# Kernel optimization log

Hardware: AMD Instinct MI355X
Metric: run time of the kernel (lower is better)

The kernel has to match this reference:

```python
import jax, jax.numpy as jnp
import numpy as np

D_MODEL = 1024
NUM_HEADS = 16
D_K = D_MODEL // NUM_HEADS
D_FF = 4096
LN_EPS = 1e-5


def layer_norm(x, gamma, beta):
    mu = jnp.mean(x, axis=-1, keepdims=True)
    var = jnp.var(x, axis=-1, keepdims=True)
    return (x - mu) * jax.lax.rsqrt(var + LN_EPS) * gamma + beta


def setup_inputs() -> dict:
    key = jax.random.key(0)
    ks = jax.random.split(key, 10)
    s = 0.02
    return {
        "x": jax.random.normal(ks[0], (2, 2048, D_MODEL), dtype=jnp.float32),
        # per-head projections stacked: [H, d_model, d_k] (equivalent to the
        # num_heads separate nn.Linear(d_model, d_k, bias=False) modules)
        "Wq": jax.random.normal(ks[1], (NUM_HEADS, D_MODEL, D_K), dtype=jnp.float32) * s,
        "Wk": jax.random.normal(ks[2], (NUM_HEADS, D_MODEL, D_K), dtype=jnp.float32) * s,
        "Wv": jax.random.normal(ks[3], (NUM_HEADS, D_MODEL, D_K), dtype=jnp.float32) * s,
        "Wo": jax.random.normal(ks[4], (D_MODEL, D_MODEL), dtype=jnp.float32) * s,
        "W1": jax.random.normal(ks[5], (D_MODEL, D_FF), dtype=jnp.float32) * s,
        "b1": jnp.zeros((D_FF,), dtype=jnp.float32),
        "W2": jax.random.normal(ks[6], (D_FF, D_MODEL), dtype=jnp.float32) * s,
        "b2": jnp.zeros((D_MODEL,), dtype=jnp.float32),
        "g1": jnp.ones((D_MODEL,), dtype=jnp.float32),
        "beta1": jnp.zeros((D_MODEL,), dtype=jnp.float32),
        "g2": jnp.ones((D_MODEL,), dtype=jnp.float32),
        "beta2": jnp.zeros((D_MODEL,), dtype=jnp.float32),
    }


def reference(x, Wq, Wk, Wv, Wo, W1, b1, W2, b2, g1, beta1, g2, beta2):
    B, S, D = x.shape
    # ---- pre-LN multi-head self-attention ----
    h = layer_norm(x, g1, beta1)
    # batched QKV projections (equivalent to the per-head Python loop)
    Q = jnp.einsum('bsd,hdk->bhsk', h, Wq)  # [B,H,S,dk]
    K = jnp.einsum('bsd,hdk->bhsk', h, Wk)
    V = jnp.einsum('bsd,hdk->bhsk', h, Wv)
    scores = jnp.einsum('bhqk,bhsk->bhqs', Q, K) / jnp.sqrt(jnp.asarray(D_K, x.dtype))
    weights = jax.nn.softmax(scores, axis=-1)  # [B,H,S,S]
    attn = jnp.einsum('bhqs,bhsk->bhqk', weights, V)  # [B,H,S,dk]
    # concat heads along feature dim (head order preserved)
    concat = attn.transpose(0, 2, 1, 3).reshape(B, S, D)
    x = x + concat @ Wo
    # ---- pre-LN FFN (exact erf GELU, matching nn.GELU default) ----
    h2 = layer_norm(x, g2, beta2)
    ffn = jax.nn.gelu(h2 @ W1 + b1, approximate=False) @ W2 + b2
    return x + ffn
```

## Files before the change

### kernel.cpp

```cpp
#include <hip/hip_runtime.h>
#include <stdint.h>


typedef __attribute__((ext_vector_type(8))) short bf16x8;
typedef __attribute__((ext_vector_type(4))) float f32x4;
typedef __attribute__((ext_vector_type(16))) float f32x16;
typedef __attribute__((ext_vector_type(4))) unsigned short u16x4;
typedef __attribute__((ext_vector_type(4))) unsigned int u32x4;

#define DEV __device__ __forceinline__

static constexpr int DM   = 1024;
static constexpr int DFF  = 4096;
static constexpr int NH   = 16;
static constexpr int DKH  = 64;
static constexpr int SEQ  = 2048;
static constexpr int NBAT = 2;
static constexpr int NTOK = NBAT * SEQ;

DEV unsigned short f2bf(float f) {
  union { float f; unsigned int u; } v; v.f = f;
  unsigned int u = v.u;
  return (unsigned short)((u + 0x7fffu + ((u >> 16) & 1u)) >> 16);
}

DEV void gload_lds16(const unsigned short* g, unsigned short* l) {
  __builtin_amdgcn_global_load_lds(
      (const __attribute__((address_space(1))) unsigned int*)g,
      (__attribute__((address_space(3))) unsigned int*)l, 16, 0, 0);
}

DEV float fast_gelu(float x) {
  const float z = fabsf(x) * 0.70710678118654752f;
  const float t = __builtin_amdgcn_rcpf(1.0f + 0.3275911f * z);
  float p = 1.061405429f;
  p = p * t - 1.453152027f;
  p = p * t + 1.421413741f;
  p = p * t - 0.284496736f;
  p = p * t + 0.254829592f;
  p = p * t;
  float erfv = 1.0f - p * __expf(-z * z);
  erfv = copysignf(erfv, x);
  return 0.5f * x * (1.0f + erfv);
}

__global__ __launch_bounds__(256) void ln_kernel(
    const float* __restrict__ x, const float* __restrict__ g,
    const float* __restrict__ be, unsigned short* __restrict__ out) {
  const int row = blockIdx.x;
  const int t = threadIdx.x;
  const int lane = t & 63, w = t >> 6;
  const float4* xr = (const float4*)(x + (size_t)row * DM);
  float4 v = xr[t];
  float s  = v.x + v.y + v.z + v.w;
  float s2 = v.x * v.x + v.y * v.y + v.z * v.z + v.w * v.w;
#pragma unroll
  for (int off = 32; off; off >>= 1) {
    s  += __shfl_down(s, off);
    s2 += __shfl_down(s2, off);
  }
  __shared__ float rs_[4], rq_[4];
  if (lane == 0) { rs_[w] = s; rq_[w] = s2; }
  __syncthreads();
  float fs = rs_[0] + rs_[1] + rs_[2] + rs_[3];
  float fq = rq_[0] + rq_[1] + rq_[2] + rq_[3];
  float mu = fs * (1.0f / DM);
  float var = fq * (1.0f / DM) - mu * mu;
  float rstd = rsqrtf(var + 1e-5f);
  float4 gv = ((const float4*)g)[t];
  float4 bv = ((const float4*)be)[t];
  u16x4 o;
  o[0] = f2bf((v.x - mu) * rstd * gv.x + bv.x);
  o[1] = f2bf((v.y - mu) * rstd * gv.y + bv.y);
  o[2] = f2bf((v.z - mu) * rstd * gv.z + bv.z);
  o[3] = f2bf((v.w - mu) * rstd * gv.w + bv.w);
  *(u16x4*)(out + (size_t)row * DM + t * 4) = o;
}

__global__ __launch_bounds__(256) void transpose_weights(
    const float* __restrict__ Wq, const float* __restrict__ Wk,
    const float* __restrict__ Wv, const float* __restrict__ Wo,
    const float* __restrict__ W1, const float* __restrict__ W2,
    unsigned short* __restrict__ wqkv_t, unsigned short* __restrict__ wo_t,
    unsigned short* __restrict__ w1_t, unsigned short* __restrict__ w2_t) {
  __shared__ float lds[64][65];
  const int t = blockIdx.x;
  const float* inb; unsigned short* outb; int in_ld, out_ld;
  if (t < 768) {
    const int slice = t >> 4, tin = t & 15;
    const int which = slice >> 4, h = slice & 15;
    const float* W = (which == 0) ? Wq : (which == 1) ? Wk : Wv;
    inb = W + (size_t)((h << 10) + (tin << 6)) * 64;
    in_ld = 64;
    outb = wqkv_t + ((size_t)((which << 10) + (h << 6)) << 10) + (tin << 6);
    out_ld = 1024;
  } else if (t < 1024) {
    const int tt = t - 768, tr = tt >> 4, tc = tt & 15;
    inb = Wo + (size_t)(tc << 6) * 1024 + (tr << 6); in_ld = 1024;
    outb = wo_t + (size_t)(tr << 6) * 1024 + (tc << 6); out_ld = 1024;
  } else if (t < 2048) {
    const int tt = t - 1024, tr = tt >> 4, tc = tt & 15;
    inb = W1 + (size_t)(tc << 6) * 4096 + (tr << 6); in_ld = 4096;
    outb = w1_t + (size_t)(tr << 6) * 1024 + (tc << 6); out_ld = 1024;
  } else {
    const int tt = t - 2048, tr = tt >> 6, tc = tt & 63;
    inb = W2 + (size_t)(tc << 6) * 1024 + (tr << 6); in_ld = 1024;
    outb = w2_t + (size_t)(tr << 6) * 4096 + (tc << 6); out_ld = 4096;
  }
  const int j = threadIdx.x & 63, i0 = threadIdx.x >> 6;
#pragma unroll
  for (int p = 0; p < 16; ++p) {
    const int i = i0 + p * 4;
    lds[j][i] = inb[(size_t)i * in_ld + j];
  }
  __syncthreads();
#pragma unroll
  for (int p = 0; p < 16; ++p) {
    const int r = i0 + p * 4;
    outb[(size_t)r * out_ld + j] = f2bf(lds[r][j]);
  }
}

struct EpiArgs {
  unsigned short* q;
  unsigned short* k;
  unsigned short* vt;
  unsigned short* ob16;
  float* of32;
  float* p0;
  const float* bias;
  const float* resid;
};

template <int EPI>
DEV void epilogue_elem(float v, int row, int col, int N, int bz,
                       const EpiArgs& ep) {
  if constexpr (EPI == 0) {
    const int bb = row >> 11, rr = row & 2047;
    if (col < 1024) {
      const int hh = col >> 6, dk = col & 63;
      const int kk = dk >> 4, h8 = (dk >> 3) & 1, e = dk & 7;
      const int qblk = rr >> 5, l31 = rr & 31;
      ep.q[((size_t)(bb * NH + hh) * 64 + qblk) * 2048 + kk * 512 +
           (h8 * 32 + l31) * 8 + e] = f2bf(v * 0.18033688011112042f);
    } else if (col < 2048) {
      const int c = col - 1024;
      const int hh = c >> 6, dk = c & 63;
      const int kk = dk >> 4, h8 = (dk >> 3) & 1, e = dk & 7;
      const int kvblk = rr >> 5, l31 = rr & 31;
      ep.k[((size_t)(bb * NH + hh) * 64 + kvblk) * 2048 + kk * 512 +
           (h8 * 32 + l31) * 8 + e] = f2bf(v);
    } else {
      const int c = col - 2048, hh = c >> 6, dd = c & 63;
      const int ssw = (rr & ~12) | ((rr & 4) << 1) | ((rr & 8) >> 1);
      const int t64 = ssw >> 6, w = (ssw >> 4) & 3;
      const int h8 = (ssw >> 3) & 1, e = ssw & 7;
      const int dblk = dd >> 5, l31 = dd & 31;
      ep.vt[(((size_t)(bb * NH + hh) * 32 + t64) * 8 + dblk * 4 + w) * 512 +
            (h8 * 32 + l31) * 8 + e] = f2bf(v);
    }
  } else if constexpr (EPI == 1) {
    const size_t idx = (size_t)row * N + col;
    ep.of32[idx] = v + ep.resid[idx];
  } else if constexpr (EPI == 2) {
    ep.ob16[(size_t)row * N + col] = f2bf(fast_gelu(v + ep.bias[col]));
  } else {
    const size_t idx = (size_t)row * N + col;
    if (bz == 0) ep.p0[idx] = v;
    else ep.of32[idx] = ep.of32[idx] + v + ep.bias[col];
  }
}

template <int EPI>
__global__ __launch_bounds__(512, 2) void gemm_256(
    const unsigned short* __restrict__ A, const unsigned short* __restrict__ Bt,
    int N, int K, int ldk, EpiArgs ep) {
  __shared__ __align__(16) unsigned short Als[2][256 * 64];
  __shared__ __align__(16) unsigned short Bls[2][256 * 64];
  const int t = threadIdx.x, lane = t & 63, wave = t >> 6;
  const int wm = wave >> 2, wn = wave & 3;
  const int g = lane >> 4, r16 = lane & 15;
  const int nx = gridDim.x, nwg = nx * gridDim.y;
  int wgid = blockIdx.y * nx + blockIdx.x;
  wgid = (wgid & 7) * (nwg >> 3) + (wgid >> 3);
  const int m0 = (wgid / nx) * 256, n0 = (wgid % nx) * 256;

  f32x4 acc[8][4];
  const f32x4 z4 = {0.f, 0.f, 0.f, 0.f};
#pragma unroll
  for (int i = 0; i < 8; ++i)
#pragma unroll
    for (int j = 0; j < 4; ++j) acc[i][j] = z4;

  auto stage_half = [&](int b, int k0, int h) {
#pragma unroll
    for (int i = 0; i < 2; ++i) {
      const int c = i * 512 + t;
      const int row = c >> 3;
      const int sc = ((c & 7) ^ (row & 7)) * 8;
      const int dofs = ((h & 1) << 13) + (i * 512 + (wave << 6)) * 8;
      if (h < 2)
        gload_lds16(A + (size_t)(m0 + ((h & 1) << 7) + row) * ldk + k0 + sc,
                    &Als[b][dofs]);
      else
        gload_lds16(Bt + (size_t)(n0 + ((h & 1) << 7) + row) * ldk + k0 + sc,
                    &Bls[b][dofs]);
    }
  };

  const int NT = K >> 6;
#pragma unroll
  for (int h = 0; h < 4; ++h) stage_half(0, 0, h);

  for (int kt = 0; kt < NT; ++kt) {
    const int cur = kt & 1;
    const bool more = (kt + 1) < NT;
    const int nk0 = (kt + 1) << 6;
    __builtin_amdgcn_s_barrier();
    if (more) {
      stage_half(cur ^ 1, nk0, 0);
      stage_half(cur ^ 1, nk0, 1);
      asm volatile("s_waitcnt vmcnt(4)" ::: "memory");
    } else {
      asm volatile("s_waitcnt vmcnt(0)" ::: "memory");
    }
    __builtin_amdgcn_s_barrier();
    __builtin_amdgcn_sched_barrier(0);

    bf16x8 Af[8][2];
#pragma unroll
    for (int mf = 0; mf < 8; ++mf) {
      const int row = (wm << 7) + (mf << 4) + r16;
#pragma unroll
      for (int ks = 0; ks < 2; ++ks)
        Af[mf][ks] = *(const bf16x8*)
            &Als[cur][row * 64 + ((((ks << 2) | g) ^ (row & 7)) << 3)];
    }
#pragma unroll
    for (int qn = 0; qn < 2; ++qn) {
      bf16x8 Bf[2][2];
#pragma unroll
      for (int ni = 0; ni < 2; ++ni) {
        const int row = (wn << 6) + (((qn << 1) | ni) << 4) + r16;
#pragma unroll
        for (int ks = 0; ks < 2; ++ks)
          Bf[ni][ks] = *(const bf16x8*)
              &Bls[cur][row * 64 + ((((ks << 2) | g) ^ (row & 7)) << 3)];
      }
      __builtin_amdgcn_s_setprio(1);
#pragma unroll
      for (int ks = 0; ks < 2; ++ks)
#pragma unroll
        for (int mf = 0; mf < 8; ++mf)
#pragma unroll
          for (int ni = 0; ni < 2; ++ni)
            acc[mf][(qn << 1) | ni] = __builtin_amdgcn_mfma_f32_16x16x32_bf16(
                Af[mf][ks], Bf[ni][ks], acc[mf][(qn << 1) | ni], 0, 0, 0);
      __builtin_amdgcn_s_setprio(0);
      if (qn == 0 && more) {
        stage_half(cur ^ 1, nk0, 2);
        stage_half(cur ^ 1, nk0, 3);
      }
    }
  }
#pragma unroll
  for (int mf = 0; mf < 8; ++mf)
#pragma unroll
    for (int nf = 0; nf < 4; ++nf)
#pragma unroll
      for (int r = 0; r < 4; ++r)
        epilogue_elem<EPI>(acc[mf][nf][r],
                           m0 + (wm << 7) + (mf << 4) + (g << 2) + r,
                           n0 + (wn << 6) + (nf << 4) + r16, N, 0, ep);
}

template <int EPI>
__global__ __launch_bounds__(256) void gemm_pipe(
    const unsigned short* __restrict__ A, const unsigned short* __restrict__ Bt,
    int N, int Kc, int ldk, EpiArgs ep) {
  __shared__ __align__(16) unsigned short Als[2][128 * 64];
  __shared__ __align__(16) unsigned short Bls[2][128 * 64];
  const int t = threadIdx.x, lane = t & 63, wave = t >> 6;
  const int wm = wave >> 1, wn = wave & 1;
  const int g = lane >> 4, r16 = lane & 15;
  const int nx = gridDim.x;
  const int nwg = nx * gridDim.y;
  int wgid = blockIdx.y * nx + blockIdx.x;
  wgid = (wgid & 7) * (nwg >> 3) + (wgid >> 3);
  const int m0 = (wgid / nx) * 128, n0 = (wgid % nx) * 128;
  const int kbase = blockIdx.z * Kc;

  f32x4 acc[4][4];
  const f32x4 z4 = {0.f, 0.f, 0.f, 0.f};
#pragma unroll
  for (int i = 0; i < 4; ++i)
#pragma unroll
    for (int j = 0; j < 4; ++j) acc[i][j] = z4;

  auto stage = [&](int b, int k0) {
#pragma unroll
    for (int i = 0; i < 4; ++i) {
      const int cb = i * 256 + wave * 64;
      const int c = cb + lane;
      const int row = c >> 3;
      const int sc = ((c & 7) ^ (row & 7)) * 8;
      gload_lds16(A + (size_t)(m0 + row) * ldk + kbase + k0 + sc, &Als[b][cb * 8]);
      gload_lds16(Bt + (size_t)(n0 + row) * ldk + kbase + k0 + sc, &Bls[b][cb * 8]);
    }
  };

  const int NT = Kc >> 6;
  stage(0, 0);
  for (int kt = 0; kt < NT; ++kt) {
    const int cur = kt & 1;
    __builtin_amdgcn_s_barrier();
    if (kt + 1 < NT) {
      stage(cur ^ 1, (kt + 1) << 6);
      asm volatile("s_waitcnt vmcnt(8)" ::: "memory");
    } else {
      asm volatile("s_waitcnt vmcnt(0)" ::: "memory");
    }
    __builtin_amdgcn_s_barrier();
    __builtin_amdgcn_sched_barrier(0);

    const int sw = r16 & 7;
    bf16x8 af[2][4], bfr[2][4];
#pragma unroll
    for (int ks = 0; ks < 2; ++ks) {
#pragma unroll
      for (int mt = 0; mt < 4; ++mt)
        af[ks][mt] = *(const bf16x8*)&Als[cur][(wm * 64 + mt * 16 + r16) * 64 +
                                              (((ks << 2) | g) ^ sw) * 8];
#pragma unroll
      for (int nt = 0; nt < 4; ++nt)
        bfr[ks][nt] = *(const bf16x8*)&Bls[cur][(wn * 64 + nt * 16 + r16) * 64 +
                                               (((ks << 2) | g) ^ sw) * 8];
    }
    __builtin_amdgcn_s_setprio(1);
#pragma unroll
    for (int ks = 0; ks < 2; ++ks)
#pragma unroll
      for (int mt = 0; mt < 4; ++mt)
#pragma unroll
        for (int nt = 0; nt < 4; ++nt)
          acc[mt][nt] = __builtin_amdgcn_mfma_f32_16x16x32_bf16(
              af[ks][mt], bfr[ks][nt], acc[mt][nt], 0, 0, 0);
    __builtin_amdgcn_s_setprio(0);
  }
#pragma unroll
  for (int mt = 0; mt < 4; ++mt)
#pragma unroll
    for (int nt = 0; nt < 4; ++nt)
#pragma unroll
      for (int r = 0; r < 4; ++r)
        epilogue_elem<EPI>(acc[mt][nt][r], m0 + wm * 64 + mt * 16 + g * 4 + r,
                           n0 + wn * 64 + nt * 16 + r16, N, blockIdx.z, ep);
}

__global__ __launch_bounds__(256) void reduce_add(const float* __restrict__ p,
                                                  float* __restrict__ out) {
  const int i = blockIdx.x * 256 + threadIdx.x;
  float4 a = ((const float4*)p)[i];
  float4 b = ((float4*)out)[i];
  b.x += a.x; b.y += a.y; b.z += a.z; b.w += a.w;
  ((float4*)out)[i] = b;
}

struct AttnState {
  f32x16 o0, o1;
  float m, lsum;
};

DEV void load_k(const unsigned short* kbase, int s, bf16x8 k0[4], bf16x8 k1[4]) {
  const unsigned short* p = kbase + (size_t)(s >> 5) * 2048;
#pragma unroll
  for (int kk = 0; kk < 4; ++kk) {
    k0[kk] = *(const bf16x8*)(p + kk * 512);
    k1[kk] = *(const bf16x8*)(p + 2048 + kk * 512);
  }
}

DEV void attn_tile(const bf16x8 k0[4], const bf16x8 k1[4],
                   const bf16x8 v0[4], const bf16x8 v1[4],
                   const bf16x8 qf[4], AttnState& st) {
  const f32x16 z16 = {0.f};
  f32x16 pA = z16, pB = z16;
  __builtin_amdgcn_s_setprio(1);
#pragma unroll
  for (int kk = 0; kk < 4; ++kk) {
    pA = __builtin_amdgcn_mfma_f32_32x32x16_bf16(k0[kk], qf[kk], pA, 0, 0, 0);
    pB = __builtin_amdgcn_mfma_f32_32x32x16_bf16(k1[kk], qf[kk], pB, 0, 0, 0);
  }
  __builtin_amdgcn_s_setprio(0);
  float m0 = fmaxf(pA[0], pB[0]), m1 = fmaxf(pA[1], pB[1]);
  float m2 = fmaxf(pA[2], pB[2]), m3 = fmaxf(pA[3], pB[3]);
#pragma unroll
  for (int r = 4; r < 16; r += 4) {
    m0 = fmaxf(m0, fmaxf(pA[r + 0], pB[r + 0]));
    m1 = fmaxf(m1, fmaxf(pA[r + 1], pB[r + 1]));
    m2 = fmaxf(m2, fmaxf(pA[r + 2], pB[r + 2]));
    m3 = fmaxf(m3, fmaxf(pA[r + 3], pB[r + 3]));
  }
  float mx = fmaxf(fmaxf(m0, m1), fmaxf(m2, m3));
  mx = fmaxf(mx, __shfl_xor(mx, 32));
  if (__any(mx > st.m + 11.5416f)) {
    const float mnew = fmaxf(st.m, mx);
    const float corr = __builtin_amdgcn_exp2f(st.m - mnew);
#pragma unroll
    for (int r = 0; r < 16; ++r) { st.o0[r] *= corr; st.o1[r] *= corr; }
    st.lsum *= corr;
    st.m = mnew;
  }
  float ps = 0.f;
#pragma unroll
  for (int r = 0; r < 16; ++r) {
    pA[r] = __builtin_amdgcn_exp2f(pA[r] - st.m); ps += pA[r];
    pB[r] = __builtin_amdgcn_exp2f(pB[r] - st.m); ps += pB[r];
  }
  ps += __shfl_xor(ps, 32);
  st.lsum += ps;
  bf16x8 pw[4];
#pragma unroll
  for (int w = 0; w < 4; ++w) {
    unsigned int wd0, wd1, wd2, wd3;
    const int e0 = (w & 1) * 8;
    if (w < 2) {
      asm("v_cvt_pk_bf16_f32 %0, %1, %2" : "=v"(wd0) : "v"(pA[e0 + 0]), "v"(pA[e0 + 1]));
      asm("v_cvt_pk_bf16_f32 %0, %1, %2" : "=v"(wd1) : "v"(pA[e0 + 2]), "v"(pA[e0 + 3]));
      asm("v_cvt_pk_bf16_f32 %0, %1, %2" : "=v"(wd2) : "v"(pA[e0 + 4]), "v"(pA[e0 + 5]));
      asm("v_cvt_pk_bf16_f32 %0, %1, %2" : "=v"(wd3) : "v"(pA[e0 + 6]), "v"(pA[e0 + 7]));
    } else {
      asm("v_cvt_pk_bf16_f32 %0, %1, %2" : "=v"(wd0) : "v"(pB[e0 + 0]), "v"(pB[e0 + 1]));
      asm("v_cvt_pk_bf16_f32 %0, %1, %2" : "=v"(wd1) : "v"(pB[e0 + 2]), "v"(pB[e0 + 3]));
      asm("v_cvt_pk_bf16_f32 %0, %1, %2" : "=v"(wd2) : "v"(pB[e0 + 4]), "v"(pB[e0 + 5]));
      asm("v_cvt_pk_bf16_f32 %0, %1, %2" : "=v"(wd3) : "v"(pB[e0 + 6]), "v"(pB[e0 + 7]));
    }
    u32x4 wv = {wd0, wd1, wd2, wd3};
    pw[w] = __builtin_bit_cast(bf16x8, wv);
  }
  __builtin_amdgcn_s_setprio(1);
#pragma unroll
  for (int w = 0; w < 4; ++w) {
    st.o0 = __builtin_amdgcn_mfma_f32_32x32x16_bf16(v0[w], pw[w], st.o0, 0, 0, 0);
    st.o1 = __builtin_amdgcn_mfma_f32_32x32x16_bf16(v1[w], pw[w], st.o1, 0, 0, 0);
  }
  __builtin_amdgcn_s_setprio(0);
}

__global__ __launch_bounds__(256, 2) void attn_kernel(
    const unsigned short* __restrict__ Qc, const unsigned short* __restrict__ Kc,
    const unsigned short* __restrict__ Vt, unsigned short* __restrict__ Oc) {
  const int lane = threadIdx.x & 63, wave = threadIdx.x >> 6;
  const int hi = lane >> 5, l31 = lane & 31;
  const int i = blockIdx.x;
  const int k8 = i & 7, mq = i >> 3;
  const int grp = k8 + 8 * (mq >> 4);
  const int qb = mq & 15;
  const int b = grp >> 4, h = grp & 15;
  const int q0 = qb * 128 + wave * 32;

  const unsigned short* qbp = Qc + ((size_t)grp * 64 + (q0 >> 5)) * 2048 + lane * 8;
  const unsigned short* kbp = Kc + (size_t)grp * 64 * 2048 + lane * 8;
  const unsigned short* vbp = Vt + (size_t)grp * 32 * 4096 + lane * 8;

  bf16x8 qf[4];
#pragma unroll
  for (int kk = 0; kk < 4; ++kk) qf[kk] = *(const bf16x8*)(qbp + kk * 512);

  AttnState st;
#pragma unroll
  for (int r = 0; r < 16; ++r) { st.o0[r] = 0.f; st.o1[r] = 0.f; }
  st.m = -1e30f; st.lsum = 0.f;

  bf16x8 kA0[4], kA1[4], kB0[4], kB1[4];
  load_k(kbp, 0, kA0, kA1);

  for (int s0 = 0; s0 < SEQ; s0 += 128) {
    const unsigned short* vt0 = vbp + (size_t)(s0 >> 6) * 4096;
    bf16x8 v0[4], v1[4];
#pragma unroll
    for (int w = 0; w < 4; ++w) {
      v0[w] = *(const bf16x8*)(vt0 + w * 512);
      v1[w] = *(const bf16x8*)(vt0 + 2048 + w * 512);
    }
    load_k(kbp, s0 + 64, kB0, kB1);
    attn_tile(kA0, kA1, v0, v1, qf, st);
    const unsigned short* vt1 = vbp + (size_t)((s0 + 64) >> 6) * 4096;
#pragma unroll
    for (int w = 0; w < 4; ++w) {
      v0[w] = *(const bf16x8*)(vt1 + w * 512);
      v1[w] = *(const bf16x8*)(vt1 + 2048 + w * 512);
    }
    const int snext = (s0 + 128 < SEQ) ? (s0 + 128) : 0;
    load_k(kbp, snext, kA0, kA1);
    attn_tile(kB0, kB1, v0, v1, qf, st);
  }

  const float inv = 1.0f / st.lsum;
  const size_t rowbase = (size_t)b * SEQ;
  unsigned short* op = Oc + (rowbase + q0 + l31) * DM + h * DKH + hi * 4;
#pragma unroll
  for (int dblk = 0; dblk < 2; ++dblk)
#pragma unroll
    for (int g4 = 0; g4 < 4; ++g4) {
      u16x4 stv;
#pragma unroll
      for (int r = 0; r < 4; ++r) {
        const float v = (dblk ? st.o1[g4 * 4 + r] : st.o0[g4 * 4 + r]) * inv;
        stv[r] = f2bf(v);
      }
      *(u16x4*)(op + dblk * 32 + g4 * 8) = stv;
    }
}

extern "C" void kernel_launch(void* const* d_in, const int* in_sizes, int n_in,
                              void* d_out, int out_size, void* d_ws,
                              size_t ws_size, hipStream_t stream) {
  (void)in_sizes; (void)n_in; (void)out_size; (void)ws_size;
  const float* x   = (const float*)d_in[0];
  const float* Wq  = (const float*)d_in[1];
  const float* Wk  = (const float*)d_in[2];
  const float* Wv  = (const float*)d_in[3];
  const float* Wo  = (const float*)d_in[4];
  const float* W1  = (const float*)d_in[5];
  const float* b1  = (const float*)d_in[6];
  const float* W2  = (const float*)d_in[7];
  const float* b2  = (const float*)d_in[8];
  const float* g1  = (const float*)d_in[9];
  const float* be1 = (const float*)d_in[10];
  const float* g2  = (const float*)d_in[11];
  const float* be2 = (const float*)d_in[12];
  float* out = (float*)d_out;

  char* ws = (char*)d_ws;
  const size_t MB = 1024 * 1024;
  unsigned short* h_buf  = (unsigned short*)(ws + 0 * MB);
  unsigned short* wqkv_t = (unsigned short*)(ws + 8 * MB);
  unsigned short* wo_t   = (unsigned short*)(ws + 14 * MB);
  unsigned short* w1_t   = (unsigned short*)(ws + 16 * MB);
  unsigned short* w2_t   = (unsigned short*)(ws + 24 * MB);
  unsigned short* q_attn = (unsigned short*)(ws + 32 * MB);
  unsigned short* k_attn = (unsigned short*)(ws + 40 * MB);
  unsigned short* v_attn = (unsigned short*)(ws + 48 * MB);
  unsigned short* ffn1   = (unsigned short*)(ws + 32 * MB);
  float*          p0     = (float*)(ws + 0 * MB);

  EpiArgs e0 = {}; e0.q = q_attn; e0.k = k_attn; e0.vt = v_attn;
  EpiArgs e1 = {}; e1.of32 = out; e1.resid = x;
  EpiArgs e2 = {}; e2.ob16 = ffn1; e2.bias = b1;
  EpiArgs e4 = {}; e4.of32 = out; e4.p0 = p0; e4.bias = b2;

  transpose_weights<<<3072, 256, 0, stream>>>(Wq, Wk, Wv, Wo, W1, W2,
                                              wqkv_t, wo_t, w1_t, w2_t);
  ln_kernel<<<NTOK, 256, 0, stream>>>(x, g1, be1, h_buf);
  gemm_256<0><<<dim3(3072 / 256, NTOK / 256), 512, 0, stream>>>(
      h_buf, wqkv_t, 3072, DM, DM, e0);
  attn_kernel<<<512, 256, 0, stream>>>(q_attn, k_attn, v_attn, h_buf);
  gemm_pipe<1><<<dim3(DM / 128, NTOK / 128, 1), 256, 0, stream>>>(
      h_buf, wo_t, DM, DM, DM, e1);
  ln_kernel<<<NTOK, 256, 0, stream>>>(out, g2, be2, h_buf);
  gemm_256<2><<<dim3(DFF / 256, NTOK / 256), 512, 0, stream>>>(
      h_buf, w1_t, DFF, DM, DM, e2);
  gemm_pipe<4><<<dim3(DM / 128, NTOK / 128, 2), 256, 0, stream>>>(
      ffn1, w2_t, DM, DFF / 2, DFF, e4);
  reduce_add<<<4096, 256, 0, stream>>>(p0, out);
}
```

Measured before the change: 255.0 us.

## Split FFN down-projection four ways on 256-tile GEMM with bf16 partials; fuse LN1 into prep

The second FFN GEMM moves from the 128-tile kernel with 2-way split-K to the 256-tile kernel with 4-way split-K. Three slices write bf16 partials, the last slice accumulates directly into the output, and a new reduce kernel sums the partials. The first LayerNorm is folded into the weight-transpose launch to save a kernel launch and let the two overlap. This is meant to raise GEMM efficiency and occupancy for the K=4096 GEMM and cut partial-sum traffic. In exchange it stores partials in reduced precision, which adds rounding error to the FFN output.

After: 273.1 us. +7.1%, slower.

```diff
diff --git a/kernel.cpp b/kernel.cpp
--- a/kernel.cpp
+++ b/kernel.cpp
@@ -17,11 +17,17 @@
 static constexpr int SEQ  = 2048;
 static constexpr int NBAT = 2;
 static constexpr int NTOK = NBAT * SEQ;
+static constexpr size_t SLAB = 4194304;
 
 DEV unsigned short f2bf(float f) {
   union { float f; unsigned int u; } v; v.f = f;
   unsigned int u = v.u;
   return (unsigned short)((u + 0x7fffu + ((u >> 16) & 1u)) >> 16);
+}
+
+DEV float bf2f(unsigned short s) {
+  union { unsigned int u; float f; } v; v.u = ((unsigned int)s) << 16;
+  return v.f;
 }
 
 DEV void gload_lds16(const unsigned short* g, unsigned short* l) {
@@ -44,10 +50,9 @@
   return 0.5f * x * (1.0f + erfv);
 }
 
-__global__ __launch_bounds__(256) void ln_kernel(
-    const float* __restrict__ x, const float* __restrict__ g,
-    const float* __restrict__ be, unsigned short* __restrict__ out) {
-  const int row = blockIdx.x;
+DEV void ln_body(const float* __restrict__ x, const float* __restrict__ g,
+                 const float* __restrict__ be, unsigned short* __restrict__ out,
+                 int row, float* rs_, float* rq_) {
   const int t = threadIdx.x;
   const int lane = t & 63, w = t >> 6;
   const float4* xr = (const float4*)(x + (size_t)row * DM);
@@ -59,7 +64,6 @@
     s  += __shfl_down(s, off);
     s2 += __shfl_down(s2, off);
   }
-  __shared__ float rs_[4], rq_[4];
   if (lane == 0) { rs_[w] = s; rq_[w] = s2; }
   __syncthreads();
   float fs = rs_[0] + rs_[1] + rs_[2] + rs_[3];
@@ -77,14 +81,28 @@
   *(u16x4*)(out + (size_t)row * DM + t * 4) = o;
 }
 
-__global__ __launch_bounds__(256) void transpose_weights(
+__global__ __launch_bounds__(256) void ln_kernel(
+    const float* __restrict__ x, const float* __restrict__ g,
+    const float* __restrict__ be, unsigned short* __restrict__ out) {
+  __shared__ float rs_[4], rq_[4];
+  ln_body(x, g, be, out, blockIdx.x, rs_, rq_);
+}
+
+__global__ __launch_bounds__(256) void prep_kernel(
+    const float* __restrict__ x, const float* __restrict__ g1,
+    const float* __restrict__ be1, unsigned short* __restrict__ lnout,
     const float* __restrict__ Wq, const float* __restrict__ Wk,
     const float* __restrict__ Wv, const float* __restrict__ Wo,
     const float* __restrict__ W1, const float* __restrict__ W2,
     unsigned short* __restrict__ wqkv_t, unsigned short* __restrict__ wo_t,
     unsigned short* __restrict__ w1_t, unsigned short* __restrict__ w2_t) {
   __shared__ float lds[64][65];
+  __shared__ float rs_[4], rq_[4];
   const int t = blockIdx.x;
+  if (t >= 3072) {
+    ln_body(x, g1, be1, lnout, t - 3072, rs_, rq_);
+    return;
+  }
   const float* inb; unsigned short* outb; int in_ld, out_ld;
   if (t < 768) {
     const int slice = t >> 4, tin = t & 15;
@@ -126,8 +144,8 @@
   unsigned short* k;
   unsigned short* vt;
   unsigned short* ob16;
+  unsigned short* pb16;
   float* of32;
-  float* p0;
   const float* bias;
   const float* resid;
 };
@@ -166,7 +184,7 @@
     ep.ob16[(size_t)row * N + col] = f2bf(fast_gelu(v + ep.bias[col]));
   } else {
     const size_t idx = (size_t)row * N + col;
-    if (bz == 0) ep.p0[idx] = v;
+    if (bz < 3) ep.pb16[(size_t)bz * SLAB + idx] = f2bf(v);
     else ep.of32[idx] = ep.of32[idx] + v + ep.bias[col];
   }
 }
@@ -174,7 +192,7 @@
 template <int EPI>
 __global__ __launch_bounds__(512, 2) void gemm_256(
     const unsigned short* __restrict__ A, const unsigned short* __restrict__ Bt,
-    int N, int K, int ldk, EpiArgs ep) {
+    int N, int Kc, int ldk, EpiArgs ep) {
   __shared__ __align__(16) unsigned short Als[2][256 * 64];
   __shared__ __align__(16) unsigned short Bls[2][256 * 64];
   const int t = threadIdx.x, lane = t & 63, wave = t >> 6;
@@ -184,6 +202,7 @@
   int wgid = blockIdx.y * nx + blockIdx.x;
   wgid = (wgid & 7) * (nwg >> 3) + (wgid >> 3);
   const int m0 = (wgid / nx) * 256, n0 = (wgid % nx) * 256;
+  const int kbase = blockIdx.z * Kc;
 
   f32x4 acc[8][4];
   const f32x4 z4 = {0.f, 0.f, 0.f, 0.f};
@@ -200,15 +219,15 @@
       const int sc = ((c & 7) ^ (row & 7)) * 8;
       const int dofs = ((h & 1) << 13) + (i * 512 + (wave << 6)) * 8;
       if (h < 2)
-        gload_lds16(A + (size_t)(m0 + ((h & 1) << 7) + row) * ldk + k0 + sc,
+        gload_lds16(A + (size_t)(m0 + ((h & 1) << 7) + row) * ldk + kbase + k0 + sc,
                     &Als[b][dofs]);
       else
-        gload_lds16(Bt + (size_t)(n0 + ((h & 1) << 7) + row) * ldk + k0 + sc,
+        gload_lds16(Bt + (size_t)(n0 + ((h & 1) << 7) + row) * ldk + kbase + k0 + sc,
                     &Bls[b][dofs]);
     }
   };
 
-  const int NT = K >> 6;
+  const int NT = Kc >> 6;
 #pragma unroll
   for (int h = 0; h < 4; ++h) stage_half(0, 0, h);
 
@@ -271,7 +290,7 @@
       for (int r = 0; r < 4; ++r)
         epilogue_elem<EPI>(acc[mf][nf][r],
                            m0 + (wm << 7) + (mf << 4) + (g << 2) + r,
-                           n0 + (wn << 6) + (nf << 4) + r16, N, 0, ep);
+                           n0 + (wn << 6) + (nf << 4) + r16, N, blockIdx.z, ep);
 }
 
 template <int EPI>
@@ -357,13 +376,18 @@
                            n0 + wn * 64 + nt * 16 + r16, N, blockIdx.z, ep);
 }
 
-__global__ __launch_bounds__(256) void reduce_add(const float* __restrict__ p,
-                                                  float* __restrict__ out) {
-  const int i = blockIdx.x * 256 + threadIdx.x;
-  float4 a = ((const float4*)p)[i];
-  float4 b = ((float4*)out)[i];
-  b.x += a.x; b.y += a.y; b.z += a.z; b.w += a.w;
-  ((float4*)out)[i] = b;
+__global__ __launch_bounds__(256) void reduce3(
+    const unsigned short* __restrict__ pb, float* __restrict__ out) {
+  const size_t i = (size_t)(blockIdx.x * 256 + threadIdx.x);
+  u16x4 a = *(const u16x4*)(pb + i * 4);
+  u16x4 b = *(const u16x4*)(pb + SLAB + i * 4);
+  u16x4 c = *(const u16x4*)(pb + 2 * SLAB + i * 4);
+  float4 o = ((float4*)out)[i];
+  o.x += bf2f(a[0]) + bf2f(b[0]) + bf2f(c[0]);
+  o.y += bf2f(a[1]) + bf2f(b[1]) + bf2f(c[1]);
+  o.z += bf2f(a[2]) + bf2f(b[2]) + bf2f(c[2]);
+  o.w += bf2f(a[3]) + bf2f(b[3]) + bf2f(c[3]);
+  ((float4*)out)[i] = o;
 }
 
 struct AttnState {
@@ -543,25 +567,24 @@
   unsigned short* k_attn = (unsigned short*)(ws + 40 * MB);
   unsigned short* v_attn = (unsigned short*)(ws + 48 * MB);
   unsigned short* ffn1   = (unsigned short*)(ws + 32 * MB);
-  float*          p0     = (float*)(ws + 0 * MB);
+  unsigned short* pb16   = (unsigned short*)(ws + 0 * MB);
 
   EpiArgs e0 = {}; e0.q = q_attn; e0.k = k_attn; e0.vt = v_attn;
   EpiArgs e1 = {}; e1.of32 = out; e1.resid = x;
   EpiArgs e2 = {}; e2.ob16 = ffn1; e2.bias = b1;
-  EpiArgs e4 = {}; e4.of32 = out; e4.p0 = p0; e4.bias = b2;
-
-  transpose_weights<<<3072, 256, 0, stream>>>(Wq, Wk, Wv, Wo, W1, W2,
-                                              wqkv_t, wo_t, w1_t, w2_t);
-  ln_kernel<<<NTOK, 256, 0, stream>>>(x, g1, be1, h_buf);
-  gemm_256<0><<<dim3(3072 / 256, NTOK / 256), 512, 0, stream>>>(
+  EpiArgs e5 = {}; e5.of32 = out; e5.pb16 = pb16; e5.bias = b2;
+
+  prep_kernel<<<3072 + NTOK, 256, 0, stream>>>(
+      x, g1, be1, h_buf, Wq, Wk, Wv, Wo, W1, W2, wqkv_t, wo_t, w1_t, w2_t);
+  gemm_256<0><<<dim3(3072 / 256, NTOK / 256, 1), 512, 0, stream>>>(
       h_buf, wqkv_t, 3072, DM, DM, e0);
   attn_kernel<<<512, 256, 0, stream>>>(q_attn, k_attn, v_attn, h_buf);
   gemm_pipe<1><<<dim3(DM / 128, NTOK / 128, 1), 256, 0, stream>>>(
       h_buf, wo_t, DM, DM, DM, e1);
   ln_kernel<<<NTOK, 256, 0, stream>>>(out, g2, be2, h_buf);
-  gemm_256<2><<<dim3(DFF / 256, NTOK / 256), 512, 0, stream>>>(
+  gemm_256<2><<<dim3(DFF / 256, NTOK / 256, 1), 512, 0, stream>>>(
       h_buf, w1_t, DFF, DM, DM, e2);
-  gemm_pipe<4><<<dim3(DM / 128, NTOK / 128, 2), 256, 0, stream>>>(
-      ffn1, w2_t, DM, DFF / 2, DFF, e4);
-  reduce_add<<<4096, 256, 0, stream>>>(p0, out);
-}
+  gemm_256<5><<<dim3(DM / 256, NTOK / 256, 4), 512, 0, stream>>>(
+      ffn1, w2_t, DM, DFF / 4, DFF, e5);
+  reduce3<<<4096, 256, 0, stream>>>(pb16, out);
+}
```
